# Optimization experiments

Hardware: AMD Instinct MI355X
Metric: run time of the kernel (lower is better)

The kernel has to match this reference:

```python
import jax, jax.numpy as jnp
import numpy as np
import math

TAU = 2.0
V_THRESHOLD = 1.0
ALPHA = 5.0  # surrogate-gradient sharpness


@jax.custom_vjp
def spike(x):
    # Heaviside step: 1.0 where x > 0 else 0.0
    return (x > 0).astype(x.dtype)


def _spike_fwd(x):
    return spike(x), x


def _spike_bwd(x, g):
    # SurrGradSpike backward: alpha/2 / (1 + (pi/2 * alpha * x)^2) * g
    scaled = (math.pi / 2.0) * ALPHA * x
    return ((ALPHA / 2.0) / (1.0 + scaled * scaled) * g,)


spike.defvjp(_spike_fwd, _spike_bwd)


def setup_inputs() -> dict:
    key = jax.random.key(0)
    T, B, N = 100, 256, 2048
    inputs = jax.random.normal(key, (T, B, N), dtype=jnp.float32)
    return {"inputs": inputs}


def reference(inputs) -> jnp.ndarray:
    # LIF neuron recurrence with synaptic current delayed by one step.
    # inputs: [T, B, N]; output spikes: [T, B, N]
    T, B, N = inputs.shape
    decay = 1.0 - 1.0 / TAU

    def step(carry, h1):
        mem, syn = carry
        mthr = mem - V_THRESHOLD
        out = spike(mthr)
        rst = jax.lax.stop_gradient(out)  # detach_reset=True
        new_mem = (decay * mem + syn) * (1.0 - rst)
        return (new_mem, h1), out

    init = (jnp.zeros((B, N), dtype=inputs.dtype),
            jnp.zeros((B, N), dtype=inputs.dtype))
    _, spk = jax.lax.scan(step, init, inputs)
    return spk  # [T, B, N], matches torch stack(dim=1).permute(1,0,2)
```

## Files before the change

### kernel.cpp

```cpp
#include <hip/hip_runtime.h>


constexpr int T_STEPS = 100;

__global__ __launch_bounds__(256) void lif_kernel(const float4* __restrict__ in,
                                                  float4* __restrict__ out,
                                                  int bn4) {
    const int i = blockIdx.x * blockDim.x + threadIdx.x;
    if (i >= bn4) return;

    float4 mem = make_float4(0.f, 0.f, 0.f, 0.f);
    float4 syn = make_float4(0.f, 0.f, 0.f, 0.f);

    const float4* __restrict__ ip = in + i;
    float4* __restrict__ op = out + i;

#pragma unroll 4
    for (int t = 0; t < T_STEPS; ++t) {
        float4 h = ip[(long)t * bn4];

        float4 o;
        o.x = mem.x > 1.0f ? 1.0f : 0.0f;
        o.y = mem.y > 1.0f ? 1.0f : 0.0f;
        o.z = mem.z > 1.0f ? 1.0f : 0.0f;
        o.w = mem.w > 1.0f ? 1.0f : 0.0f;

        mem.x = (o.x != 0.0f) ? 0.0f : fmaf(0.5f, mem.x, syn.x);
        mem.y = (o.y != 0.0f) ? 0.0f : fmaf(0.5f, mem.y, syn.y);
        mem.z = (o.z != 0.0f) ? 0.0f : fmaf(0.5f, mem.z, syn.z);
        mem.w = (o.w != 0.0f) ? 0.0f : fmaf(0.5f, mem.w, syn.w);

        syn = h;

        op[(long)t * bn4] = o;
    }
}

extern "C" void kernel_launch(void* const* d_in, const int* in_sizes, int n_in,
                              void* d_out, int out_size, void* d_ws, size_t ws_size,
                              hipStream_t stream) {
    const float* in = (const float*)d_in[0];
    float* out = (float*)d_out;

    const int total = in_sizes[0];
    const int bn = total / T_STEPS;
    const int bn4 = bn / 4;

    const int block = 256;
    const int grid = (bn4 + block - 1) / block;

    lif_kernel<<<grid, block, 0, stream>>>((const float4*)in, (float4*)out, bn4);
}
```

Before: 341.8 us.

## Use float2 per thread with nontemporal loads/stores and two-step prefetch

Result: faster. 330.9 us (-3.2%).

```diff
diff --git a/kernel.cpp b/kernel.cpp
--- a/kernel.cpp
+++ b/kernel.cpp
@@ -3,36 +3,42 @@
 
 constexpr int T_STEPS = 100;
 
-__global__ __launch_bounds__(256) void lif_kernel(const float4* __restrict__ in,
-                                                  float4* __restrict__ out,
-                                                  int bn4) {
+typedef float v2f __attribute__((ext_vector_type(2)));
+
+__global__ __launch_bounds__(256) void lif_kernel(const v2f* __restrict__ in,
+                                                  v2f* __restrict__ out,
+                                                  int bn2) {
     const int i = blockIdx.x * blockDim.x + threadIdx.x;
-    if (i >= bn4) return;
+    if (i >= bn2) return;
 
-    float4 mem = make_float4(0.f, 0.f, 0.f, 0.f);
-    float4 syn = make_float4(0.f, 0.f, 0.f, 0.f);
+    const v2f* __restrict__ ip = in + i;
+    v2f* __restrict__ op = out + i;
 
-    const float4* __restrict__ ip = in + i;
-    float4* __restrict__ op = out + i;
+    v2f mem = 0.0f;
+    v2f syn = 0.0f;
 
-#pragma unroll 4
+    v2f hA = __builtin_nontemporal_load(ip);
+    v2f hB = __builtin_nontemporal_load(ip + (long)bn2);
+
+#pragma unroll
     for (int t = 0; t < T_STEPS; ++t) {
-        float4 h = ip[(long)t * bn4];
+        v2f hn = 0.0f;
+        if (t + 2 < T_STEPS) {
+            hn = __builtin_nontemporal_load(ip + (long)(t + 2) * bn2);
+        }
 
-        float4 o;
+        v2f o;
         o.x = mem.x > 1.0f ? 1.0f : 0.0f;
         o.y = mem.y > 1.0f ? 1.0f : 0.0f;
-        o.z = mem.z > 1.0f ? 1.0f : 0.0f;
-        o.w = mem.w > 1.0f ? 1.0f : 0.0f;
+
+        __builtin_nontemporal_store(o, op + (long)t * bn2);
 
         mem.x = (o.x != 0.0f) ? 0.0f : fmaf(0.5f, mem.x, syn.x);
         mem.y = (o.y != 0.0f) ? 0.0f : fmaf(0.5f, mem.y, syn.y);
-        mem.z = (o.z != 0.0f) ? 0.0f : fmaf(0.5f, mem.z, syn.z);
-        mem.w = (o.w != 0.0f) ? 0.0f : fmaf(0.5f, mem.w, syn.w);
 
-        syn = h;
-
-        op[(long)t * bn4] = o;
+        syn = hA;
+        hA = hB;
+        hB = hn;
     }
 }
 
@@ -44,10 +50,10 @@
 
     const int total = in_sizes[0];
     const int bn = total / T_STEPS;
-    const int bn4 = bn / 4;
+    const int bn2 = bn / 2;
 
     const int block = 256;
-    const int grid = (bn4 + block - 1) / block;
+    const int grid = (bn2 + block - 1) / block;
 
-    lif_kernel<<<grid, block, 0, stream>>>((const float4*)in, (float4*)out, bn4);
+    lif_kernel<<<grid, block, 0, stream>>>((const v2f*)in, (v2f*)out, bn2);
 }
```
